# Optimization experiments

Measured on AMD Instinct MI355X. Metric: run time of the kernel, lower is better.

Reference implementation:

```python
import jax, jax.numpy as jnp
import numpy as np

# anchor encoding indices: [x,y,z,log w,log l,log h,sin,cos,vx,vy,vz]
NUM_HEADS = 8
LN_EPS = 1e-5


def layer_norm(x, g, b):
    mu = jnp.mean(x, axis=-1, keepdims=True)
    var = jnp.var(x, axis=-1, keepdims=True)
    return (x - mu) * jax.lax.rsqrt(var + LN_EPS) * g + b


def align_anchors_to_frame(anchor, Tm):
    # anchor: (..., N, 11), Tm: (..., 4, 4)
    R = Tm[..., :3, :3]
    t = Tm[..., :3, 3]
    center = jnp.einsum('...ij,...nj->...ni', R, anchor[..., 0:3]) + t[..., None, :]
    size = anchor[..., 3:6]
    yaw = jnp.einsum('...ij,...nj->...ni', R[..., :2, :2], anchor[..., 6:8])
    vel = jnp.einsum('...ij,...nj->...ni', R, anchor[..., 8:11])
    return jnp.concatenate([center, size, yaw, vel], axis=-1)


def setup_inputs() -> dict:
    key = jax.random.key(0)
    ks = jax.random.split(key, 12)
    B, T, N, C, E, A = 2, 12, 1024, 256, 256, 11
    inp = {
        'seq_features': jax.random.normal(ks[0], (B, T, N, C), jnp.float32),
        'seq_anchors': jax.random.normal(ks[1], (B, T, N, A), jnp.float32),
        'T_ego_his2cur': jax.random.normal(ks[2], (B, T, 4, 4), jnp.float32),
        'Wf': jax.random.normal(ks[3], (E, C), jnp.float32) * (C ** -0.5),
        'bf': jnp.zeros((E,), jnp.float32),
        'Wa': jax.random.normal(ks[4], (E, A), jnp.float32) * (A ** -0.5),
        'ba': jnp.zeros((E,), jnp.float32),
        'Win': jax.random.normal(ks[5], (3 * E, E), jnp.float32) * (E ** -0.5),
        'bin_': jnp.zeros((3 * E,), jnp.float32),
        'gamma': jnp.ones((E,), jnp.float32),
        'beta': jnp.zeros((E,), jnp.float32),
    }
    return inp


def reference(seq_features, seq_anchors, T_ego_his2cur, Wf, bf, Wa, ba, Win, bin_, gamma, beta):
    B, T, N, C = seq_features.shape
    E = gamma.shape[0]
    H = NUM_HEADS
    D = E // H

    feat_cur = seq_features[:, 1:]    # (B,T-1,N,C)
    feat_prev = seq_features[:, :-1]
    anc_cur = seq_anchors[:, 1:]
    anc_prev = align_anchors_to_frame(seq_anchors[:, :-1], T_ego_his2cur[:, 1:])

    tok_cur = layer_norm(feat_cur @ Wf.T + bf + anc_cur @ Wa.T + ba, gamma, beta)
    tok_prev = layer_norm(feat_prev @ Wf.T + bf + anc_prev @ Wa.T + ba, gamma, beta)

    Wq, Wk = Win[:E], Win[E:2 * E]
    bq, bk = bin_[:E], bin_[E:2 * E]
    scale = np.float32(D) ** np.float32(-0.5)
    q = ((tok_cur @ Wq.T + bq) * scale).reshape(B, T - 1, N, H, D)
    k = (tok_prev @ Wk.T + bk).reshape(B, T - 1, N, H, D)

    scores = jnp.einsum('btnhd,btmhd->bthnm', q, k)  # (B,T-1,H,N,N)
    attn = jax.nn.softmax(scores, axis=-1).mean(axis=2)  # head-averaged weights

    eye = jnp.broadcast_to(jnp.eye(N, dtype=seq_features.dtype), (B, 1, N, N))
    return jnp.concatenate([eye, attn], axis=1)  # (B,T,N,N)
```

## Files before the change

### kernel.cpp

```cpp
#include <hip/hip_runtime.h>
#include <hip/hip_bf16.h>
#include <math.h>

#define LN_EPS 1e-5f

typedef short bf16x8 __attribute__((ext_vector_type(8)));
typedef float f32x4 __attribute__((ext_vector_type(4)));

__device__ inline short f2bf(float f) {
  union { float f; unsigned u; } v; v.f = f;
  unsigned r = v.u + 0x7FFFu + ((v.u >> 16) & 1u);
  return (short)(r >> 16);
}
__device__ inline float bf2f(unsigned short s) {
  union { unsigned u; float f; } v; v.u = ((unsigned)s) << 16;
  return v.f;
}
__device__ inline float fast_exp2(float x) {
#if __has_builtin(__builtin_amdgcn_exp2f)
  return __builtin_amdgcn_exp2f(x);
#else
  return __expf(x * 0.69314718056f);
#endif
}

__global__ __launch_bounds__(256) void gemm_feat(const float* __restrict__ Ap,
    const float* __restrict__ W, const float* __restrict__ bias,
    short* __restrict__ Out)
{
  __shared__ short lda[64][40];
  __shared__ short ldb[64][40];
  const int tid = threadIdx.x;
  const int bm = blockIdx.x * 64, bn = blockIdx.y * 64;
  const int wid = tid >> 6, lane = tid & 63;
  const int quad = lane >> 4, l15 = lane & 15;
  const int wm = (wid & 1) * 32, wn = (wid >> 1) * 32;
  const int srow = tid >> 2, sseg = tid & 3;

  f32x4 z = {0.f, 0.f, 0.f, 0.f};
  f32x4 acc[2][2];
  acc[0][0] = z; acc[0][1] = z; acc[1][0] = z; acc[1][1] = z;

  for (int kk = 0; kk < 256; kk += 32) {
    {
      const float* ap = Ap + (size_t)(bm + srow) * 256 + kk + sseg * 8;
      f32x4 x0 = *(const f32x4*)ap;
      f32x4 x1 = *(const f32x4*)(ap + 4);
      bf16x8 vv;
      vv[0] = f2bf(x0[0]); vv[1] = f2bf(x0[1]); vv[2] = f2bf(x0[2]); vv[3] = f2bf(x0[3]);
      vv[4] = f2bf(x1[0]); vv[5] = f2bf(x1[1]); vv[6] = f2bf(x1[2]); vv[7] = f2bf(x1[3]);
      *(bf16x8*)&lda[srow][sseg * 8] = vv;
    }
    {
      const float* wp = W + (size_t)(bn + srow) * 256 + kk + sseg * 8;
      f32x4 x0 = *(const f32x4*)wp;
      f32x4 x1 = *(const f32x4*)(wp + 4);
      bf16x8 vv;
      vv[0] = f2bf(x0[0]); vv[1] = f2bf(x0[1]); vv[2] = f2bf(x0[2]); vv[3] = f2bf(x0[3]);
      vv[4] = f2bf(x1[0]); vv[5] = f2bf(x1[1]); vv[6] = f2bf(x1[2]); vv[7] = f2bf(x1[3]);
      *(bf16x8*)&ldb[srow][sseg * 8] = vv;
    }
    __syncthreads();
    bf16x8 af0 = *(const bf16x8*)&lda[wm + l15][quad * 8];
    bf16x8 af1 = *(const bf16x8*)&lda[wm + 16 + l15][quad * 8];
    bf16x8 bq0 = *(const bf16x8*)&ldb[wn + l15][quad * 8];
    bf16x8 bq1 = *(const bf16x8*)&ldb[wn + 16 + l15][quad * 8];
    acc[0][0] = __builtin_amdgcn_mfma_f32_16x16x32_bf16(af0, bq0, acc[0][0], 0, 0, 0);
    acc[0][1] = __builtin_amdgcn_mfma_f32_16x16x32_bf16(af0, bq1, acc[0][1], 0, 0, 0);
    acc[1][0] = __builtin_amdgcn_mfma_f32_16x16x32_bf16(af1, bq0, acc[1][0], 0, 0, 0);
    acc[1][1] = __builtin_amdgcn_mfma_f32_16x16x32_bf16(af1, bq1, acc[1][1], 0, 0, 0);
    __syncthreads();
  }

  #pragma unroll
  for (int i = 0; i < 2; ++i)
    #pragma unroll
    for (int j = 0; j < 2; ++j)
      #pragma unroll
      for (int r = 0; r < 4; ++r) {
        int grow = bm + wm + i * 16 + quad * 4 + r;
        int gcol = bn + wn + j * 16 + l15;
        Out[(size_t)grow * 256 + gcol] = f2bf(acc[i][j][r] + bias[gcol]);
      }
}

__global__ __launch_bounds__(256) void gemm_qk(const short* __restrict__ tokc,
    const short* __restrict__ tokp, const float* __restrict__ Win,
    const float* __restrict__ binv, short* __restrict__ qb, short* __restrict__ kb)
{
  const int sel = blockIdx.z;
  const short* Ap = sel ? tokp : tokc;
  const float* W = Win + (size_t)sel * 65536;
  const float* bias = binv + sel * 256;
  const float alpha = sel ? 1.0f : 0.17677669529663687f * 1.4426950408889634f;
  short* Out = sel ? kb : qb;

  __shared__ short lda[64][40];
  __shared__ short ldb[64][40];
  const int tid = threadIdx.x;
  const int bm = blockIdx.x * 64, bn = blockIdx.y * 64;
  const int wid = tid >> 6, lane = tid & 63;
  const int quad = lane >> 4, l15 = lane & 15;
  const int wm = (wid & 1) * 32, wn = (wid >> 1) * 32;
  const int srow = tid >> 2, sseg = tid & 3;

  f32x4 z = {0.f, 0.f, 0.f, 0.f};
  f32x4 acc[2][2];
  acc[0][0] = z; acc[0][1] = z; acc[1][0] = z; acc[1][1] = z;

  for (int kk = 0; kk < 256; kk += 32) {
    *(bf16x8*)&lda[srow][sseg * 8] =
        *(const bf16x8*)(Ap + (size_t)(bm + srow) * 256 + kk + sseg * 8);
    {
      const float* wp = W + (size_t)(bn + srow) * 256 + kk + sseg * 8;
      f32x4 x0 = *(const f32x4*)wp;
      f32x4 x1 = *(const f32x4*)(wp + 4);
      bf16x8 vv;
      vv[0] = f2bf(x0[0]); vv[1] = f2bf(x0[1]); vv[2] = f2bf(x0[2]); vv[3] = f2bf(x0[3]);
      vv[4] = f2bf(x1[0]); vv[5] = f2bf(x1[1]); vv[6] = f2bf(x1[2]); vv[7] = f2bf(x1[3]);
      *(bf16x8*)&ldb[srow][sseg * 8] = vv;
    }
    __syncthreads();
    bf16x8 af0 = *(const bf16x8*)&lda[wm + l15][quad * 8];
    bf16x8 af1 = *(const bf16x8*)&lda[wm + 16 + l15][quad * 8];
    bf16x8 bq0 = *(const bf16x8*)&ldb[wn + l15][quad * 8];
    bf16x8 bq1 = *(const bf16x8*)&ldb[wn + 16 + l15][quad * 8];
    acc[0][0] = __builtin_amdgcn_mfma_f32_16x16x32_bf16(af0, bq0, acc[0][0], 0, 0, 0);
    acc[0][1] = __builtin_amdgcn_mfma_f32_16x16x32_bf16(af0, bq1, acc[0][1], 0, 0, 0);
    acc[1][0] = __builtin_amdgcn_mfma_f32_16x16x32_bf16(af1, bq0, acc[1][0], 0, 0, 0);
    acc[1][1] = __builtin_amdgcn_mfma_f32_16x16x32_bf16(af1, bq1, acc[1][1], 0, 0, 0);
    __syncthreads();
  }

  #pragma unroll
  for (int i = 0; i < 2; ++i)
    #pragma unroll
    for (int j = 0; j < 2; ++j)
      #pragma unroll
      for (int r = 0; r < 4; ++r) {
        int grow = bm + wm + i * 16 + quad * 4 + r;
        int gcol = bn + wn + j * 16 + l15;
        float v = (acc[i][j][r] + bias[gcol]) * alpha;
        int btr = grow >> 10, nn = grow & 1023, h = gcol >> 5, d = gcol & 31;
        Out[(((size_t)btr * 8 + h) * 1024 + nn) * 32 + d] = f2bf(v);
      }
}

__global__ __launch_bounds__(256) void anchor_ln(const short* __restrict__ featproj,
  const float* __restrict__ anchors, const float* __restrict__ Tego,
  const float* __restrict__ Wa, const float* __restrict__ ba,
  const float* __restrict__ gamma, const float* __restrict__ beta,
  short* __restrict__ tok_cur, short* __restrict__ tok_prev)
{
  const int wid = threadIdx.x >> 6, lane = threadIdx.x & 63;
  const int tok = blockIdx.x * 4 + wid;
  const int which = tok >= 22528 ? 1 : 0;
  const int rem = tok - which * 22528;
  const int bt = rem >> 10;
  const int n = rem & 1023;
  const int b = bt / 11, t = bt - b * 11;
  const int tt = which ? t : t + 1;

  const float* ap = anchors + (((size_t)b * 12 + tt) * 1024 + n) * 11;
  float a[11];
  #pragma unroll
  for (int j = 0; j < 11; ++j) a[j] = ap[j];
  if (which) {
    const float* Tm = Tego + ((size_t)b * 12 + t + 1) * 16;
    float r00 = Tm[0], r01 = Tm[1], r02 = Tm[2],  t0 = Tm[3];
    float r10 = Tm[4], r11 = Tm[5], r12 = Tm[6],  t1 = Tm[7];
    float r20 = Tm[8], r21 = Tm[9], r22 = Tm[10], t2 = Tm[11];
    float a0 = a[0], a1 = a[1], a2 = a[2];
    float a6 = a[6], a7 = a[7], a8 = a[8], a9 = a[9], a10 = a[10];
    a[0] = r00 * a0 + r01 * a1 + r02 * a2 + t0;
    a[1] = r10 * a0 + r11 * a1 + r12 * a2 + t1;
    a[2] = r20 * a0 + r21 * a1 + r22 * a2 + t2;
    a[6] = r00 * a6 + r01 * a7;
    a[7] = r10 * a6 + r11 * a7;
    a[8] = r00 * a8 + r01 * a9 + r02 * a10;
    a[9] = r10 * a8 + r11 * a9 + r12 * a10;
    a[10] = r20 * a8 + r21 * a9 + r22 * a10;
  }

  const int c0 = lane * 4;
  const size_t frow = (((size_t)b * 12 + tt) * 1024 + n) * 256 + c0;
  ushort4 raw = *(const ushort4*)(featproj + frow);
  f32x4 bav = *(const f32x4*)(ba + c0);
  float v[4];
  v[0] = bf2f(raw.x) + bav[0]; v[1] = bf2f(raw.y) + bav[1];
  v[2] = bf2f(raw.z) + bav[2]; v[3] = bf2f(raw.w) + bav[3];
  #pragma unroll
  for (int c = 0; c < 4; ++c) {
    const float* war = Wa + (size_t)(c0 + c) * 11;
    float acc = 0.f;
    #pragma unroll
    for (int j = 0; j < 11; ++j) acc += war[j] * a[j];
    v[c] += acc;
  }
  float s1 = v[0] + v[1] + v[2] + v[3];
  float s2 = v[0]*v[0] + v[1]*v[1] + v[2]*v[2] + v[3]*v[3];
  #pragma unroll
  for (int off = 1; off < 64; off <<= 1) { s1 += __shfl_xor(s1, off); s2 += __shfl_xor(s2, off); }
  float mean = s1 * (1.0f / 256.0f);
  float var = s2 * (1.0f / 256.0f) - mean * mean;
  float rstd = rsqrtf(var + LN_EPS);
  f32x4 gv = *(const f32x4*)(gamma + c0);
  f32x4 bv = *(const f32x4*)(beta + c0);
  ushort4 o;
  o.x = (unsigned short)f2bf((v[0] - mean) * rstd * gv[0] + bv[0]);
  o.y = (unsigned short)f2bf((v[1] - mean) * rstd * gv[1] + bv[1]);
  o.z = (unsigned short)f2bf((v[2] - mean) * rstd * gv[2] + bv[2]);
  o.w = (unsigned short)f2bf((v[3] - mean) * rstd * gv[3] + bv[3]);
  short* dst = which ? tok_prev : tok_cur;
  *(ushort4*)(dst + ((size_t)bt * 1024 + n) * 256 + c0) = o;
}

__global__ __launch_bounds__(256) void denom_kernel(const short* __restrict__ q,
  const short* __restrict__ k, float* __restrict__ dinv)
{
  __shared__ short kst[2][4096];
  const int tid = threadIdx.x, wid = tid >> 6, lane = tid & 63;
  const int quad = lane >> 4, l15 = lane & 15;
  const int h = blockIdx.y, bt = blockIdx.z;
  const int n0 = blockIdx.x * 128 + wid * 32;
  const size_t base = ((size_t)bt * 8 + h) * 1024 * 32;
  bf16x8 qf0 = *(const bf16x8*)(q + base + (size_t)(n0 + l15) * 32 + quad * 8);
  bf16x8 qf1 = *(const bf16x8*)(q + base + (size_t)(n0 + 16 + l15) * 32 + quad * 8);
  const short* ksA = k + base + (size_t)(wid * 16) * 32 + lane * 8;
  const short* ksB = k + base + (size_t)((wid + 4) * 16) * 32 + lane * 8;
  const int wswz = ((lane & 3) ^ ((lane >> 3) & 3)) * 8;
  const int rswz = (quad ^ ((l15 >> 1) & 3)) * 8;
  short* lwA = &kst[0][wid * 512 + (lane >> 2) * 32 + wswz];
  short* lwB = &kst[0][(wid + 4) * 512 + (lane >> 2) * 32 + wswz];

  f32x4 z = {0.f, 0.f, 0.f, 0.f};
  float sum0[4] = {0.f, 0.f, 0.f, 0.f};
  float sum1[4] = {0.f, 0.f, 0.f, 0.f};

  bf16x8 stA = *(const bf16x8*)ksA;
  bf16x8 stB = *(const bf16x8*)ksB;
  *(bf16x8*)lwA = stA;
  *(bf16x8*)lwB = stB;
  __syncthreads();

  #pragma unroll 1
  for (int rd = 0; rd < 8; ++rd) {
    const int buf = rd & 1;
    if (rd < 7) {
      stA = *(const bf16x8*)(ksA + (size_t)(rd + 1) * 128 * 32);
      stB = *(const bf16x8*)(ksB + (size_t)(rd + 1) * 128 * 32);
    }
    #pragma unroll
    for (int s = 0; s < 8; ++s) {
      bf16x8 kf = *(const bf16x8*)&kst[buf][s * 512 + l15 * 32 + rswz];
      f32x4 sc0 = __builtin_amdgcn_mfma_f32_16x16x32_bf16(qf0, kf, z, 0, 0, 0);
      f32x4 sc1 = __builtin_amdgcn_mfma_f32_16x16x32_bf16(qf1, kf, z, 0, 0, 0);
      #pragma unroll
      for (int r = 0; r < 4; ++r) {
        sum0[r] += fast_exp2(sc0[r]);
        sum1[r] += fast_exp2(sc1[r]);
      }
    }
    if (rd < 7) {
      *(bf16x8*)(lwA + ((buf ^ 1) << 12)) = stA;
      *(bf16x8*)(lwB + ((buf ^ 1) << 12)) = stB;
    }
    __syncthreads();
  }
  #pragma unroll
  for (int off = 1; off < 16; off <<= 1) {
    #pragma unroll
    for (int r = 0; r < 4; ++r) {
      sum0[r] += __shfl_xor(sum0[r], off);
      sum1[r] += __shfl_xor(sum1[r], off);
    }
  }
  if (l15 == 0) {
    float* dp = dinv + ((size_t)bt * 8 + h) * 1024 + n0 + quad * 4;
    #pragma unroll
    for (int r = 0; r < 4; ++r) {
      dp[r] = 1.f / sum0[r];
      dp[16 + r] = 1.f / sum1[r];
    }
  }
}

__global__ __launch_bounds__(256) void prob_kernel(const short* __restrict__ q,
  const short* __restrict__ k, const float* __restrict__ dinv, float* __restrict__ out)
{
  __shared__ short kst[2][4096];
  const int tid = threadIdx.x, wid = tid >> 6, lane = tid & 63;
  const int quad = lane >> 4, l15 = lane & 15;
  const int bt = blockIdx.z;
  const int n0 = blockIdx.x * 64 + wid * 16;
  const int mbase = blockIdx.y * 128;
  const int b = bt / 11, t = bt - b * 11;
  bf16x8 qf[8];
  float invd[8][4];
  #pragma unroll
  for (int h = 0; h < 8; ++h) {
    const size_t base = ((size_t)bt * 8 + h) * 1024 * 32;
    qf[h] = *(const bf16x8*)(q + base + (size_t)(n0 + l15) * 32 + quad * 8);
    const float* dp = dinv + ((size_t)bt * 8 + h) * 1024 + n0 + quad * 4;
    #pragma unroll
    for (int r = 0; r < 4; ++r) invd[h][r] = dp[r] * 0.125f;
  }
  const short* ksA = k + (((size_t)bt * 8 + wid    ) * 1024 + mbase) * 32 + lane * 8;
  const short* ksB = k + (((size_t)bt * 8 + wid + 4) * 1024 + mbase) * 32 + lane * 8;
  const int wswz = ((lane & 3) ^ ((lane >> 3) & 3)) * 8;
  const int rswz = (quad ^ ((l15 >> 1) & 3)) * 8;
  short* lwA = &kst[0][wid * 512 + (lane >> 2) * 32 + wswz];
  short* lwB = &kst[0][(wid + 4) * 512 + (lane >> 2) * 32 + wswz];

  float* ob = out + ((size_t)(b * 12 + t + 1)) * 1024 * 1024
                  + (size_t)(n0 + quad * 4) * 1024 + l15;
  f32x4 z = {0.f, 0.f, 0.f, 0.f};

  bf16x8 stA = *(const bf16x8*)ksA;
  bf16x8 stB = *(const bf16x8*)ksB;
  *(bf16x8*)lwA = stA;
  *(bf16x8*)lwB = stB;
  __syncthreads();

  #pragma unroll 1
  for (int mt = 0; mt < 8; ++mt) {
    const int buf = mt & 1;
    if (mt < 7) {
      stA = *(const bf16x8*)(ksA + (size_t)(mt + 1) * 16 * 32);
      stB = *(const bf16x8*)(ksB + (size_t)(mt + 1) * 16 * 32);
    }
    float P0 = 0, P1 = 0, P2 = 0, P3 = 0;
    #pragma unroll
    for (int h = 0; h < 8; ++h) {
      bf16x8 kf = *(const bf16x8*)&kst[buf][h * 512 + l15 * 32 + rswz];
      f32x4 s = __builtin_amdgcn_mfma_f32_16x16x32_bf16(qf[h], kf, z, 0, 0, 0);
      P0 += fast_exp2(s[0]) * invd[h][0];
      P1 += fast_exp2(s[1]) * invd[h][1];
      P2 += fast_exp2(s[2]) * invd[h][2];
      P3 += fast_exp2(s[3]) * invd[h][3];
    }
    float* op = ob + mbase + mt * 16;
    op[0] = P0; op[1024] = P1; op[2048] = P2; op[3072] = P3;
    if (mt < 7) {
      *(bf16x8*)(lwA + ((buf ^ 1) << 12)) = stA;
      *(bf16x8*)(lwB + ((buf ^ 1) << 12)) = stB;
    }
    __syncthreads();
  }
}

__global__ __launch_bounds__(256) void eye_kernel(float* __restrict__ out) {
  int gid = blockIdx.x * 256 + threadIdx.x;
  int b = gid >> 18, rem = gid & 262143;
  int n = rem >> 8, m4 = rem & 255;
  f32x4 v = {0.f, 0.f, 0.f, 0.f};
  int c = n - m4 * 4;
  if (c >= 0 && c < 4) v[c] = 1.0f;
  *(f32x4*)(out + (size_t)b * 12582912 + (size_t)n * 1024 + m4 * 4) = v;
}

extern "C" void kernel_launch(void* const* d_in, const int* in_sizes, int n_in,
                              void* d_out, int out_size, void* d_ws, size_t ws_size,
                              hipStream_t stream)
{
  const float* sf   = (const float*)d_in[0];
  const float* sa   = (const float*)d_in[1];
  const float* te   = (const float*)d_in[2];
  const float* Wf   = (const float*)d_in[3];
  const float* bfv  = (const float*)d_in[4];
  const float* Wa   = (const float*)d_in[5];
  const float* ba   = (const float*)d_in[6];
  const float* Win  = (const float*)d_in[7];
  const float* binv = (const float*)d_in[8];
  const float* gam  = (const float*)d_in[9];
  const float* bet  = (const float*)d_in[10];
  float* out = (float*)d_out;

  char* w = (char*)d_ws;
  short* featproj = (short*)w;  w += 12582912;
  short* tok_cur  = (short*)w;  w += 11534336;
  short* tok_prev = (short*)w;  w += 11534336;
  short* qb       = (short*)w;  w += 11534336;
  short* kb       = (short*)w;  w += 11534336;
  float* dinv     = (float*)w;  w += 720896;

  gemm_feat<<<dim3(384, 4), 256, 0, stream>>>(sf, Wf, bfv, featproj);
  anchor_ln<<<dim3(11264), 256, 0, stream>>>(featproj, sa, te, Wa, ba, gam, bet, tok_cur, tok_prev);
  gemm_qk<<<dim3(352, 4, 2), 256, 0, stream>>>(tok_cur, tok_prev, Win, binv, qb, kb);
  denom_kernel<<<dim3(8, 8, 22), 256, 0, stream>>>(qb, kb, dinv);
  prob_kernel<<<dim3(16, 8, 22), 256, 0, stream>>>(qb, kb, dinv, out);
  eye_kernel<<<dim3(2048), 256, 0, stream>>>(out);
}
```

Before: 268.0 us.

## Pre-convert inputs and weights to bf16 and enlarge GEMM tiles to 128x128

Adds a separate conversion kernel that turns seq_features, Wf and the Q/K part of Win into bf16 buffers. The feature and QK GEMMs then load bf16 directly and use 128x128 block tiles, with each wave computing 4x4 MFMA fragments instead of 2x2. This cuts the repeated fp32 loads and per-tile conversions and improves operand reuse. In exchange it adds an extra pass that reads the full feature tensor and writes a bf16 copy of it, and the GEMMs launch fewer blocks.

After: 263.5 us. Within noise of the previous version (-1.7%).

```diff
diff --git a/kernel.cpp b/kernel.cpp
--- a/kernel.cpp
+++ b/kernel.cpp
@@ -24,58 +24,73 @@
 #endif
 }
 
-__global__ __launch_bounds__(256) void gemm_feat(const float* __restrict__ Ap,
-    const float* __restrict__ W, const float* __restrict__ bias,
+__global__ __launch_bounds__(256) void convert_kernel(const float* __restrict__ sf,
+    const float* __restrict__ Wf, const float* __restrict__ Win,
+    short* __restrict__ sfb, short* __restrict__ Wfb, short* __restrict__ Wqkb)
+{
+  size_t i = ((size_t)blockIdx.x * 256 + threadIdx.x) * 8;
+  const float* src;
+  short* dst;
+  if (i < 6291456) { src = sf + i; dst = sfb + i; }
+  else if (i < 6356992) { src = Wf + (i - 6291456); dst = Wfb + (i - 6291456); }
+  else { src = Win + (i - 6356992); dst = Wqkb + (i - 6356992); }
+  f32x4 x0 = *(const f32x4*)src;
+  f32x4 x1 = *(const f32x4*)(src + 4);
+  bf16x8 v;
+  v[0] = f2bf(x0[0]); v[1] = f2bf(x0[1]); v[2] = f2bf(x0[2]); v[3] = f2bf(x0[3]);
+  v[4] = f2bf(x1[0]); v[5] = f2bf(x1[1]); v[6] = f2bf(x1[2]); v[7] = f2bf(x1[3]);
+  *(bf16x8*)dst = v;
+}
+
+__global__ __launch_bounds__(256) void gemm_feat(const short* __restrict__ Ap,
+    const short* __restrict__ W, const float* __restrict__ bias,
     short* __restrict__ Out)
 {
-  __shared__ short lda[64][40];
-  __shared__ short ldb[64][40];
+  __shared__ short lda[128][40];
+  __shared__ short ldb[128][40];
   const int tid = threadIdx.x;
-  const int bm = blockIdx.x * 64, bn = blockIdx.y * 64;
+  const int bm = blockIdx.x * 128, bn = blockIdx.y * 128;
   const int wid = tid >> 6, lane = tid & 63;
   const int quad = lane >> 4, l15 = lane & 15;
-  const int wm = (wid & 1) * 32, wn = (wid >> 1) * 32;
+  const int wm = (wid & 1) * 64, wn = (wid >> 1) * 64;
   const int srow = tid >> 2, sseg = tid & 3;
 
   f32x4 z = {0.f, 0.f, 0.f, 0.f};
-  f32x4 acc[2][2];
-  acc[0][0] = z; acc[0][1] = z; acc[1][0] = z; acc[1][1] = z;
+  f32x4 acc[4][4];
+  #pragma unroll
+  for (int i = 0; i < 4; ++i)
+    #pragma unroll
+    for (int j = 0; j < 4; ++j) acc[i][j] = z;
+
+  const short* a0 = Ap + (size_t)(bm + srow) * 256 + sseg * 8;
+  const short* a1 = Ap + (size_t)(bm + srow + 64) * 256 + sseg * 8;
+  const short* b0 = W + (size_t)(bn + srow) * 256 + sseg * 8;
+  const short* b1 = W + (size_t)(bn + srow + 64) * 256 + sseg * 8;
 
   for (int kk = 0; kk < 256; kk += 32) {
-    {
-      const float* ap = Ap + (size_t)(bm + srow) * 256 + kk + sseg * 8;
-      f32x4 x0 = *(const f32x4*)ap;
-      f32x4 x1 = *(const f32x4*)(ap + 4);
-      bf16x8 vv;
-      vv[0] = f2bf(x0[0]); vv[1] = f2bf(x0[1]); vv[2] = f2bf(x0[2]); vv[3] = f2bf(x0[3]);
-      vv[4] = f2bf(x1[0]); vv[5] = f2bf(x1[1]); vv[6] = f2bf(x1[2]); vv[7] = f2bf(x1[3]);
-      *(bf16x8*)&lda[srow][sseg * 8] = vv;
-    }
-    {
-      const float* wp = W + (size_t)(bn + srow) * 256 + kk + sseg * 8;
-      f32x4 x0 = *(const f32x4*)wp;
-      f32x4 x1 = *(const f32x4*)(wp + 4);
-      bf16x8 vv;
-      vv[0] = f2bf(x0[0]); vv[1] = f2bf(x0[1]); vv[2] = f2bf(x0[2]); vv[3] = f2bf(x0[3]);
-      vv[4] = f2bf(x1[0]); vv[5] = f2bf(x1[1]); vv[6] = f2bf(x1[2]); vv[7] = f2bf(x1[3]);
-      *(bf16x8*)&ldb[srow][sseg * 8] = vv;
-    }
-    __syncthreads();
-    bf16x8 af0 = *(const bf16x8*)&lda[wm + l15][quad * 8];
-    bf16x8 af1 = *(const bf16x8*)&lda[wm + 16 + l15][quad * 8];
-    bf16x8 bq0 = *(const bf16x8*)&ldb[wn + l15][quad * 8];
-    bf16x8 bq1 = *(const bf16x8*)&ldb[wn + 16 + l15][quad * 8];
-    acc[0][0] = __builtin_amdgcn_mfma_f32_16x16x32_bf16(af0, bq0, acc[0][0], 0, 0, 0);
-    acc[0][1] = __builtin_amdgcn_mfma_f32_16x16x32_bf16(af0, bq1, acc[0][1], 0, 0, 0);
-    acc[1][0] = __builtin_amdgcn_mfma_f32_16x16x32_bf16(af1, bq0, acc[1][0], 0, 0, 0);
-    acc[1][1] = __builtin_amdgcn_mfma_f32_16x16x32_bf16(af1, bq1, acc[1][1], 0, 0, 0);
-    __syncthreads();
-  }
-
-  #pragma unroll
-  for (int i = 0; i < 2; ++i)
-    #pragma unroll
-    for (int j = 0; j < 2; ++j)
+    *(bf16x8*)&lda[srow][sseg * 8]      = *(const bf16x8*)(a0 + kk);
+    *(bf16x8*)&lda[srow + 64][sseg * 8] = *(const bf16x8*)(a1 + kk);
+    *(bf16x8*)&ldb[srow][sseg * 8]      = *(const bf16x8*)(b0 + kk);
+    *(bf16x8*)&ldb[srow + 64][sseg * 8] = *(const bf16x8*)(b1 + kk);
+    __syncthreads();
+    bf16x8 af[4], bq[4];
+    #pragma unroll
+    for (int i = 0; i < 4; ++i) {
+      af[i] = *(const bf16x8*)&lda[wm + i * 16 + l15][quad * 8];
+      bq[i] = *(const bf16x8*)&ldb[wn + i * 16 + l15][quad * 8];
+    }
+    #pragma unroll
+    for (int i = 0; i < 4; ++i)
+      #pragma unroll
+      for (int j = 0; j < 4; ++j)
+        acc[i][j] = __builtin_amdgcn_mfma_f32_16x16x32_bf16(af[i], bq[j], acc[i][j], 0, 0, 0);
+    __syncthreads();
+  }
+
+  #pragma unroll
+  for (int i = 0; i < 4; ++i)
+    #pragma unroll
+    for (int j = 0; j < 4; ++j)
       #pragma unroll
       for (int r = 0; r < 4; ++r) {
         int grow = bm + wm + i * 16 + quad * 4 + r;
@@ -85,57 +100,61 @@
 }
 
 __global__ __launch_bounds__(256) void gemm_qk(const short* __restrict__ tokc,
-    const short* __restrict__ tokp, const float* __restrict__ Win,
+    const short* __restrict__ tokp, const short* __restrict__ Wqkb,
     const float* __restrict__ binv, short* __restrict__ qb, short* __restrict__ kb)
 {
   const int sel = blockIdx.z;
   const short* Ap = sel ? tokp : tokc;
-  const float* W = Win + (size_t)sel * 65536;
+  const short* W = Wqkb + (size_t)sel * 65536;
   const float* bias = binv + sel * 256;
   const float alpha = sel ? 1.0f : 0.17677669529663687f * 1.4426950408889634f;
   short* Out = sel ? kb : qb;
 
-  __shared__ short lda[64][40];
-  __shared__ short ldb[64][40];
+  __shared__ short lda[128][40];
+  __shared__ short ldb[128][40];
   const int tid = threadIdx.x;
-  const int bm = blockIdx.x * 64, bn = blockIdx.y * 64;
+  const int bm = blockIdx.x * 128, bn = blockIdx.y * 128;
   const int wid = tid >> 6, lane = tid & 63;
   const int quad = lane >> 4, l15 = lane & 15;
-  const int wm = (wid & 1) * 32, wn = (wid >> 1) * 32;
+  const int wm = (wid & 1) * 64, wn = (wid >> 1) * 64;
   const int srow = tid >> 2, sseg = tid & 3;
 
   f32x4 z = {0.f, 0.f, 0.f, 0.f};
-  f32x4 acc[2][2];
-  acc[0][0] = z; acc[0][1] = z; acc[1][0] = z; acc[1][1] = z;
+  f32x4 acc[4][4];
+  #pragma unroll
+  for (int i = 0; i < 4; ++i)
+    #pragma unroll
+    for (int j = 0; j < 4; ++j) acc[i][j] = z;
+
+  const short* a0 = Ap + (size_t)(bm + srow) * 256 + sseg * 8;
+  const short* a1 = Ap + (size_t)(bm + srow + 64) * 256 + sseg * 8;
+  const short* b0 = W + (size_t)(bn + srow) * 256 + sseg * 8;
+  const short* b1 = W + (size_t)(bn + srow + 64) * 256 + sseg * 8;
 
   for (int kk = 0; kk < 256; kk += 32) {
-    *(bf16x8*)&lda[srow][sseg * 8] =
-        *(const bf16x8*)(Ap + (size_t)(bm + srow) * 256 + kk + sseg * 8);
-    {
-      const float* wp = W + (size_t)(bn + srow) * 256 + kk + sseg * 8;
-      f32x4 x0 = *(const f32x4*)wp;
-      f32x4 x1 = *(const f32x4*)(wp + 4);
-      bf16x8 vv;
-      vv[0] = f2bf(x0[0]); vv[1] = f2bf(x0[1]); vv[2] = f2bf(x0[2]); vv[3] = f2bf(x0[3]);
-      vv[4] = f2bf(x1[0]); vv[5] = f2bf(x1[1]); vv[6] = f2bf(x1[2]); vv[7] = f2bf(x1[3]);
-      *(bf16x8*)&ldb[srow][sseg * 8] = vv;
-    }
-    __syncthreads();
-    bf16x8 af0 = *(const bf16x8*)&lda[wm + l15][quad * 8];
-    bf16x8 af1 = *(const bf16x8*)&lda[wm + 16 + l15][quad * 8];
-    bf16x8 bq0 = *(const bf16x8*)&ldb[wn + l15][quad * 8];
-    bf16x8 bq1 = *(const bf16x8*)&ldb[wn + 16 + l15][quad * 8];
-    acc[0][0] = __builtin_amdgcn_mfma_f32_16x16x32_bf16(af0, bq0, acc[0][0], 0, 0, 0);
-    acc[0][1] = __builtin_amdgcn_mfma_f32_16x16x32_bf16(af0, bq1, acc[0][1], 0, 0, 0);
-    acc[1][0] = __builtin_amdgcn_mfma_f32_16x16x32_bf16(af1, bq0, acc[1][0], 0, 0, 0);
-    acc[1][1] = __builtin_amdgcn_mfma_f32_16x16x32_bf16(af1, bq1, acc[1][1], 0, 0, 0);
-    __syncthreads();
-  }
-
-  #pragma unroll
-  for (int i = 0; i < 2; ++i)
-    #pragma unroll
-    for (int j = 0; j < 2; ++j)
+    *(bf16x8*)&lda[srow][sseg * 8]      = *(const bf16x8*)(a0 + kk);
+    *(bf16x8*)&lda[srow + 64][sseg * 8] = *(const bf16x8*)(a1 + kk);
+    *(bf16x8*)&ldb[srow][sseg * 8]      = *(const bf16x8*)(b0 + kk);
+    *(bf16x8*)&ldb[srow + 64][sseg * 8] = *(const bf16x8*)(b1 + kk);
+    __syncthreads();
+    bf16x8 af[4], bq[4];
+    #pragma unroll
+    for (int i = 0; i < 4; ++i) {
+      af[i] = *(const bf16x8*)&lda[wm + i * 16 + l15][quad * 8];
+      bq[i] = *(const bf16x8*)&ldb[wn + i * 16 + l15][quad * 8];
+    }
+    #pragma unroll
+    for (int i = 0; i < 4; ++i)
+      #pragma unroll
+      for (int j = 0; j < 4; ++j)
+        acc[i][j] = __builtin_amdgcn_mfma_f32_16x16x32_bf16(af[i], bq[j], acc[i][j], 0, 0, 0);
+    __syncthreads();
+  }
+
+  #pragma unroll
+  for (int i = 0; i < 4; ++i)
+    #pragma unroll
+    for (int j = 0; j < 4; ++j)
       #pragma unroll
       for (int r = 0; r < 4; ++r) {
         int grow = bm + wm + i * 16 + quad * 4 + r;
@@ -383,10 +402,14 @@
   short* qb       = (short*)w;  w += 11534336;
   short* kb       = (short*)w;  w += 11534336;
   float* dinv     = (float*)w;  w += 720896;
-
-  gemm_feat<<<dim3(384, 4), 256, 0, stream>>>(sf, Wf, bfv, featproj);
+  short* sfb      = (short*)w;  w += 12582912;
+  short* Wfb      = (short*)w;  w += 131072;
+  short* Wqkb     = (short*)w;  w += 262144;
+
+  convert_kernel<<<dim3(3168), 256, 0, stream>>>(sf, Wf, Win, sfb, Wfb, Wqkb);
+  gemm_feat<<<dim3(192, 2), 256, 0, stream>>>(sfb, Wfb, bfv, featproj);
   anchor_ln<<<dim3(11264), 256, 0, stream>>>(featproj, sa, te, Wa, ba, gam, bet, tok_cur, tok_prev);
-  gemm_qk<<<dim3(352, 4, 2), 256, 0, stream>>>(tok_cur, tok_prev, Win, binv, qb, kb);
+  gemm_qk<<<dim3(176, 2, 2), 256, 0, stream>>>(tok_cur, tok_prev, Wqkb, binv, qb, kb);
   denom_kernel<<<dim3(8, 8, 22), 256, 0, stream>>>(qb, kb, dinv);
   prob_kernel<<<dim3(16, 8, 22), 256, 0, stream>>>(qb, kb, dinv, out);
   eye_kernel<<<dim3(2048), 256, 0, stream>>>(out);
```
